# Performance work log

Hardware: AMD Instinct MI355X
Metric: run time of the kernel (lower is better)

## Reference

```python
import jax, jax.numpy as jnp
import numpy as np

B, C, N = 8, 64, 4096
K, M = 20, 8  # neighbors, num_kernel
OUT_C = 64
NEG_SLOPE = 0.2


def setup_inputs() -> dict:
    key = jax.random.key(0)
    k1, k2, k3, k4, k5, k6 = jax.random.split(key, 6)
    x = jax.random.normal(k1, (B, 3, N), dtype=jnp.float32)
    feature = jax.random.normal(k2, (B, C, N), dtype=jnp.float32)
    neigh_indexs = jax.random.randint(k3, (B, N, K), 0, N, dtype=jnp.int64)
    kernels = jax.random.normal(k4, (3, M), dtype=jnp.float32)
    conv_w = jax.random.normal(k5, (OUT_C, C * M), dtype=jnp.float32) * (1.0 / np.sqrt(C * M))
    conv_b = jax.random.normal(k6, (OUT_C,), dtype=jnp.float32) * 0.01
    return {"x": x, "feature": feature, "neigh_indexs": neigh_indexs,
            "kernels": kernels, "conv_w": conv_w, "conv_b": conv_b}


def reference(x, feature, neigh_indexs, kernels, conv_w, conv_b):
    b, c, n = feature.shape
    k = K
    m = kernels.shape[1]
    idx = neigh_indexs[:, :, :k]  # dilation=1 slice, (B,N,K)
    bidx = jnp.arange(b)[:, None, None]

    xt = jnp.transpose(x, (0, 2, 1))            # (B,N,3)
    x_neighs = xt[bidx, idx]                    # (B,N,K,3) irregular gather
    x_rel = x_neighs - x_neighs[:, :, :1, :]    # relative coords to first neighbor

    # kernel projection + one_padding buffer (zeros with [0,0]=1)
    one_pad = jnp.zeros((k, m), dtype=x.dtype).at[0, 0].set(1.0)
    permatrix = jnp.einsum('bnkc,cm->bnkm', x_rel, kernels) + one_pad
    # topkmax: stable softmax over the neighbor axis (soft assignment of
    # neighbors to each of the m kernel slots)
    permatrix = jax.nn.softmax(permatrix, axis=2)  # (B,N,K,M)

    ft = jnp.transpose(feature, (0, 2, 1))      # (B,N,C)
    f_neighs = ft[bidx, idx]                    # (B,N,K,C)
    # feats (B*N,C,K) @ permatrix (B*N,K,M) -> (B*N,C,M); flatten C-major
    agg = jnp.einsum('bnkc,bnkm->bncm', f_neighs, permatrix).reshape(b, n, c * m)

    # BasicConv: 1x1 conv == dense over channel dim, then LeakyReLU(0.2)
    out = agg @ conv_w.T + conv_b               # (B,N,out_c)
    out = jax.nn.leaky_relu(out, NEG_SLOPE)
    out = jnp.transpose(out, (0, 2, 1))         # (B,out_c,N)
    return out + feature                        # residual since in_c == out_c
```

## Files before the change

kernel.cpp:

```cpp
#include <hip/hip_runtime.h>

#define BB 8
#define CC 64
#define NNN 4096
#define KK 20
#define MM 8
#define OC 64
#define CM 512

typedef __attribute__((ext_vector_type(8))) short bf16x8;
typedef __attribute__((ext_vector_type(4))) float f32x4;

__device__ __forceinline__ unsigned short f2bf(float f) {
    union { float f; unsigned int u; } v; v.f = f;
    unsigned int u = v.u;
    return (unsigned short)((u + 0x7FFFu + ((u >> 16) & 1u)) >> 16);
}
__device__ __forceinline__ float bfhi2f(unsigned int u) {
    union { unsigned int u; float f; } v; v.u = u & 0xffff0000u; return v.f;
}
__device__ __forceinline__ float bflo2f(unsigned int u) {
    union { unsigned int u; float f; } v; v.u = u << 16; return v.f;
}

__global__ __launch_bounds__(256) void prep_kernel(const float* __restrict__ feature,
                                                   const float* __restrict__ conv_w,
                                                   unsigned short* __restrict__ ftr,
                                                   unsigned short* __restrict__ Wb) {
    int blk = blockIdx.x;
    int t = threadIdx.x;
    if (blk < 512) {
        __shared__ float tile[64 * 65];
        int b = blk & 7;
        int n0 = (blk >> 3) << 6;
        const float* fb = feature + b * (CC * NNN);
        #pragma unroll
        for (int s = 0; s < 16; ++s) {
            int i = t + s * 256;
            int c = i >> 6, nn = i & 63;
            tile[c * 65 + nn] = fb[c * NNN + n0 + nn];
        }
        __syncthreads();
        unsigned short* fo = ftr + b * (NNN * CC) + n0 * CC;
        #pragma unroll
        for (int s = 0; s < 16; ++s) {
            int i = t + s * 256;
            int n = i >> 6, cc = i & 63;
            fo[n * CC + cc] = f2bf(tile[cc * 65 + n]);
        }
    } else {
        int base = (blk - 512) * 8192;
        #pragma unroll
        for (int s = 0; s < 32; ++s) {
            int i = base + t + s * 256;
            Wb[i] = f2bf(conv_w[i]);
        }
    }
}

__global__ __launch_bounds__(256, 4) void main_kernel(
    const float* __restrict__ x,
    const float* __restrict__ feature,
    const int* __restrict__ nidx,
    const float* __restrict__ kern,
    const float* __restrict__ conv_b,
    const unsigned short* __restrict__ ftr,
    const unsigned short* __restrict__ Wb,
    float* __restrict__ out)
{
    __shared__ __align__(16) union {
        struct {
            int   idx[16 * KK];
            float xn[16 * KK * 3];
            float perm[16 * KK * 10];
        } s;
        unsigned short aggA[16 * 520];
    } u;

    int t = threadIdx.x;
    int blk = blockIdx.x;
    int b = blk & 7;
    int n0 = (blk >> 3) << 4;
    int w = t >> 6, l = t & 63;

    int o = (w << 4) + (l & 15);
    int pq = (l >> 4) << 2;
    float4 fres4 = *(const float4*)(feature + ((size_t)b * CC + o) * NNN + n0 + pq);
    float bias = conv_b[o];
    int m_pre = t & 7;
    float kw0 = kern[m_pre], kw1 = kern[MM + m_pre], kw2 = kern[2 * MM + m_pre];

    const int* nb = nidx + (b * NNN + n0) * KK;
    for (int i = t; i < 16 * KK; i += 256) u.s.idx[i] = nb[i];
    __syncthreads();

    const float* xb = x + b * (3 * NNN);
    float xreg[4];
    int xslot[4];
    #pragma unroll
    for (int s = 0; s < 4; ++s) {
        int i = t + s * 256;
        xslot[s] = i;
        if (i < 960) {
            int p2 = i / 60;
            int rem = i - p2 * 60;
            int k = rem / 3;
            int c = rem - k * 3;
            xreg[s] = xb[c * NNN + u.s.idx[p2 * KK + k]];
        }
    }

    int p = t >> 4;
    int cq = (t & 15) << 2;
    const unsigned short* fb = ftr + (size_t)b * (NNN * CC);
    uint2 fr[KK];
    #pragma unroll
    for (int k = 0; k < KK; ++k)
        fr[k] = *(const uint2*)(fb + (size_t)u.s.idx[p * KK + k] * CC + cq);

    #pragma unroll
    for (int s = 0; s < 4; ++s)
        if (xslot[s] < 960) u.s.xn[xslot[s]] = xreg[s];
    __syncthreads();

    if (t < 128) {
        int pp = t >> 3;
        int m = t & 7;
        const float* xp = &u.s.xn[pp * 60];
        float bx = xp[0], by = xp[1], bz = xp[2];
        float pv[KK];
        #pragma unroll
        for (int k = 0; k < KK; ++k) {
            float dx = xp[k * 3 + 0] - bx;
            float dy = xp[k * 3 + 1] - by;
            float dz = xp[k * 3 + 2] - bz;
            pv[k] = dx * kw0 + dy * kw1 + dz * kw2;
        }
        if (m == 0) pv[0] += 1.0f;
        float mx = pv[0];
        #pragma unroll
        for (int k = 1; k < KK; ++k) mx = fmaxf(mx, pv[k]);
        float sum = 0.f;
        #pragma unroll
        for (int k = 0; k < KK; ++k) { pv[k] = __expf(pv[k] - mx); sum += pv[k]; }
        float inv = 1.0f / sum;
        #pragma unroll
        for (int k = 0; k < KK; ++k) u.s.perm[(pp * KK + k) * 10 + m] = pv[k] * inv;
    }
    __syncthreads();

    float acc[4][MM];
    #pragma unroll
    for (int ci = 0; ci < 4; ++ci)
        #pragma unroll
        for (int m = 0; m < MM; ++m) acc[ci][m] = 0.f;
    #pragma unroll
    for (int k = 0; k < KK; ++k) {
        float fv[4];
        fv[0] = bflo2f(fr[k].x); fv[1] = bfhi2f(fr[k].x);
        fv[2] = bflo2f(fr[k].y); fv[3] = bfhi2f(fr[k].y);
        const float* pr = &u.s.perm[(p * KK + k) * 10];
        float2 q0 = *(const float2*)(pr + 0);
        float2 q1 = *(const float2*)(pr + 2);
        float2 q2 = *(const float2*)(pr + 4);
        float2 q3 = *(const float2*)(pr + 6);
        float pvv[8] = {q0.x, q0.y, q1.x, q1.y, q2.x, q2.y, q3.x, q3.y};
        #pragma unroll
        for (int ci = 0; ci < 4; ++ci)
            #pragma unroll
            for (int m = 0; m < MM; ++m)
                acc[ci][m] += fv[ci] * pvv[m];
    }
    __syncthreads();

    #pragma unroll
    for (int ci = 0; ci < 4; ++ci) {
        union { bf16x8 v; unsigned short s2[8]; } pk;
        #pragma unroll
        for (int m = 0; m < MM; ++m) pk.s2[m] = f2bf(acc[ci][m]);
        *(bf16x8*)&u.aggA[p * 520 + (cq + ci) * MM] = pk.v;
    }
    __syncthreads();

    {
        int row = l & 15;
        int kg = (l >> 4) << 3;
        f32x4 acc2 = {0.f, 0.f, 0.f, 0.f};
        const unsigned short* wrow = Wb + (size_t)o * CM;
        const unsigned short* arow = u.aggA + row * 520;
        #pragma unroll
        for (int s = 0; s < 16; ++s) {
            int k = s * 32 + kg;
            bf16x8 af = *(const bf16x8*)&arow[k];
            bf16x8 bfr = *(const bf16x8*)&wrow[k];
            acc2 = __builtin_amdgcn_mfma_f32_16x16x32_bf16(af, bfr, acc2, 0, 0, 0);
        }
        float4 res;
        #pragma unroll
        for (int r = 0; r < 4; ++r) {
            float v = acc2[r] + bias;
            v = v > 0.f ? v : v * 0.2f;
            ((float*)&res)[r] = v + ((const float*)&fres4)[r];
        }
        *(float4*)(out + ((size_t)b * CC + o) * NNN + n0 + pq) = res;
    }
}

extern "C" void kernel_launch(void* const* d_in, const int* in_sizes, int n_in,
                              void* d_out, int out_size, void* d_ws, size_t ws_size,
                              hipStream_t stream) {
    const float* x        = (const float*)d_in[0];
    const float* feature  = (const float*)d_in[1];
    const int*   nidx     = (const int*)d_in[2];
    const float* kern     = (const float*)d_in[3];
    const float* conv_w   = (const float*)d_in[4];
    const float* conv_b   = (const float*)d_in[5];
    float* out = (float*)d_out;

    unsigned short* ftr = (unsigned short*)d_ws;
    unsigned short* Wb  = (unsigned short*)((char*)d_ws + 4194304);

    prep_kernel<<<516, 256, 0, stream>>>(feature, conv_w, ftr, Wb);
    main_kernel<<<2048, 256, 0, stream>>>(x, feature, nidx, kern, conv_b, ftr, Wb, out);
}
```

Measured before the change: 106.7 us.

## Process 32 points per block, reuse weight fragments across two MFMA tiles

Each block now handles 32 points instead of 16, and the grid is halved. Each thread processes two points, and every conv-weight fragment loaded from global memory feeds two MFMA tiles, which halves weight traffic per point. Neighbor indices are read straight into registers with int4 loads instead of being staged in shared memory, and the second point's feature gather is issued after the softmax stage to overlap latency. The cost is higher register and LDS use, so the occupancy hint drops to 3 blocks, and with 1024 blocks there are fewer waves to hide gather latency.

```diff
diff --git a/kernel.cpp b/kernel.cpp
--- a/kernel.cpp
+++ b/kernel.cpp
@@ -7,6 +7,8 @@
 #define MM 8
 #define OC 64
 #define CM 512
+#define PTS 32
+#define AST 516
 
 typedef __attribute__((ext_vector_type(8))) short bf16x8;
 typedef __attribute__((ext_vector_type(4))) float f32x4;
@@ -58,7 +60,7 @@
     }
 }
 
-__global__ __launch_bounds__(256, 4) void main_kernel(
+__global__ __launch_bounds__(256, 3) void main_kernel(
     const float* __restrict__ x,
     const float* __restrict__ feature,
     const int* __restrict__ nidx,
@@ -70,63 +72,66 @@
 {
     __shared__ __align__(16) union {
         struct {
-            int   idx[16 * KK];
-            float xn[16 * KK * 3];
-            float perm[16 * KK * 10];
+            float xn[PTS * 60];
+            float perm[PTS * KK * 10];
         } s;
-        unsigned short aggA[16 * 520];
+        unsigned short aggA[PTS * AST];
     } u;
 
     int t = threadIdx.x;
     int blk = blockIdx.x;
     int b = blk & 7;
-    int n0 = (blk >> 3) << 4;
+    int n0 = (blk >> 3) << 5;
     int w = t >> 6, l = t & 63;
 
+    const int* nb = nidx + (b * NNN + n0) * KK;
+    const float* xb = x + b * (3 * NNN);
+    const unsigned short* fb = ftr + (size_t)b * (NNN * CC);
+
+    int p0 = t >> 4;
+    int p1 = p0 + 16;
+    int cq = (t & 15) << 2;
     int o = (w << 4) + (l & 15);
-    int pq = (l >> 4) << 2;
-    float4 fres4 = *(const float4*)(feature + ((size_t)b * CC + o) * NNN + n0 + pq);
+    int q = l >> 4;
+
+    float4 fres0 = *(const float4*)(feature + ((size_t)b * CC + o) * NNN + n0 + q * 4);
+    float4 fres1 = *(const float4*)(feature + ((size_t)b * CC + o) * NNN + n0 + 16 + q * 4);
     float bias = conv_b[o];
-    int m_pre = t & 7;
-    float kw0 = kern[m_pre], kw1 = kern[MM + m_pre], kw2 = kern[2 * MM + m_pre];
-
-    const int* nb = nidx + (b * NNN + n0) * KK;
-    for (int i = t; i < 16 * KK; i += 256) u.s.idx[i] = nb[i];
-    __syncthreads();
-
-    const float* xb = x + b * (3 * NNN);
-    float xreg[4];
-    int xslot[4];
-    #pragma unroll
-    for (int s = 0; s < 4; ++s) {
+    int mA = t & 7;
+    float kw0 = kern[mA], kw1 = kern[MM + mA], kw2 = kern[2 * MM + mA];
+
+    int id0[KK];
+    {
+        const int4* nb4 = (const int4*)(nb + p0 * KK);
+        #pragma unroll
+        for (int s = 0; s < 5; ++s) {
+            int4 v = nb4[s];
+            id0[s * 4 + 0] = v.x; id0[s * 4 + 1] = v.y;
+            id0[s * 4 + 2] = v.z; id0[s * 4 + 3] = v.w;
+        }
+    }
+    uint2 fr0[KK];
+    #pragma unroll
+    for (int k = 0; k < KK; ++k)
+        fr0[k] = *(const uint2*)(fb + (size_t)id0[k] * CC + cq);
+
+    #pragma unroll
+    for (int s = 0; s < 8; ++s) {
         int i = t + s * 256;
-        xslot[s] = i;
-        if (i < 960) {
-            int p2 = i / 60;
-            int rem = i - p2 * 60;
+        if (i < PTS * 60) {
+            int p = i / 60;
+            int rem = i - p * 60;
             int k = rem / 3;
             int c = rem - k * 3;
-            xreg[s] = xb[c * NNN + u.s.idx[p2 * KK + k]];
-        }
-    }
-
-    int p = t >> 4;
-    int cq = (t & 15) << 2;
-    const unsigned short* fb = ftr + (size_t)b * (NNN * CC);
-    uint2 fr[KK];
-    #pragma unroll
-    for (int k = 0; k < KK; ++k)
-        fr[k] = *(const uint2*)(fb + (size_t)u.s.idx[p * KK + k] * CC + cq);
-
-    #pragma unroll
-    for (int s = 0; s < 4; ++s)
-        if (xslot[s] < 960) u.s.xn[xslot[s]] = xreg[s];
-    __syncthreads();
-
-    if (t < 128) {
-        int pp = t >> 3;
-        int m = t & 7;
-        const float* xp = &u.s.xn[pp * 60];
+            int idv = nb[p * KK + k];
+            u.s.xn[i] = xb[c * NNN + idv];
+        }
+    }
+    __syncthreads();
+
+    {
+        int pA = t >> 3;
+        const float* xp = &u.s.xn[pA * 60];
         float bx = xp[0], by = xp[1], bz = xp[2];
         float pv[KK];
         #pragma unroll
@@ -136,7 +141,7 @@
             float dz = xp[k * 3 + 2] - bz;
             pv[k] = dx * kw0 + dy * kw1 + dz * kw2;
         }
-        if (m == 0) pv[0] += 1.0f;
+        if (mA == 0) pv[0] += 1.0f;
         float mx = pv[0];
         #pragma unroll
         for (int k = 1; k < KK; ++k) mx = fmaxf(mx, pv[k]);
@@ -145,21 +150,37 @@
         for (int k = 0; k < KK; ++k) { pv[k] = __expf(pv[k] - mx); sum += pv[k]; }
         float inv = 1.0f / sum;
         #pragma unroll
-        for (int k = 0; k < KK; ++k) u.s.perm[(pp * KK + k) * 10 + m] = pv[k] * inv;
-    }
-    __syncthreads();
-
-    float acc[4][MM];
+        for (int k = 0; k < KK; ++k) u.s.perm[(pA * KK + k) * 10 + mA] = pv[k] * inv;
+    }
+    __syncthreads();
+
+    int id1[KK];
+    {
+        const int4* nb4 = (const int4*)(nb + p1 * KK);
+        #pragma unroll
+        for (int s = 0; s < 5; ++s) {
+            int4 v = nb4[s];
+            id1[s * 4 + 0] = v.x; id1[s * 4 + 1] = v.y;
+            id1[s * 4 + 2] = v.z; id1[s * 4 + 3] = v.w;
+        }
+    }
+    uint2 fr1[KK];
+    #pragma unroll
+    for (int k = 0; k < KK; ++k)
+        fr1[k] = *(const uint2*)(fb + (size_t)id1[k] * CC + cq);
+
+    float acc0[4][MM], acc1[4][MM];
     #pragma unroll
     for (int ci = 0; ci < 4; ++ci)
         #pragma unroll
-        for (int m = 0; m < MM; ++m) acc[ci][m] = 0.f;
+        for (int m = 0; m < MM; ++m) { acc0[ci][m] = 0.f; acc1[ci][m] = 0.f; }
+
     #pragma unroll
     for (int k = 0; k < KK; ++k) {
         float fv[4];
-        fv[0] = bflo2f(fr[k].x); fv[1] = bfhi2f(fr[k].x);
-        fv[2] = bflo2f(fr[k].y); fv[3] = bfhi2f(fr[k].y);
-        const float* pr = &u.s.perm[(p * KK + k) * 10];
+        fv[0] = bflo2f(fr0[k].x); fv[1] = bfhi2f(fr0[k].x);
+        fv[2] = bflo2f(fr0[k].y); fv[3] = bfhi2f(fr0[k].y);
+        const float* pr = &u.s.perm[(p0 * KK + k) * 10];
         float2 q0 = *(const float2*)(pr + 0);
         float2 q1 = *(const float2*)(pr + 2);
         float2 q2 = *(const float2*)(pr + 4);
@@ -169,7 +190,24 @@
         for (int ci = 0; ci < 4; ++ci)
             #pragma unroll
             for (int m = 0; m < MM; ++m)
-                acc[ci][m] += fv[ci] * pvv[m];
+                acc0[ci][m] += fv[ci] * pvv[m];
+    }
+    #pragma unroll
+    for (int k = 0; k < KK; ++k) {
+        float fv[4];
+        fv[0] = bflo2f(fr1[k].x); fv[1] = bfhi2f(fr1[k].x);
+        fv[2] = bflo2f(fr1[k].y); fv[3] = bfhi2f(fr1[k].y);
+        const float* pr = &u.s.perm[(p1 * KK + k) * 10];
+        float2 q0 = *(const float2*)(pr + 0);
+        float2 q1 = *(const float2*)(pr + 2);
+        float2 q2 = *(const float2*)(pr + 4);
+        float2 q3 = *(const float2*)(pr + 6);
+        float pvv[8] = {q0.x, q0.y, q1.x, q1.y, q2.x, q2.y, q3.x, q3.y};
+        #pragma unroll
+        for (int ci = 0; ci < 4; ++ci)
+            #pragma unroll
+            for (int m = 0; m < MM; ++m)
+                acc1[ci][m] += fv[ci] * pvv[m];
     }
     __syncthreads();
 
@@ -177,32 +215,44 @@
     for (int ci = 0; ci < 4; ++ci) {
         union { bf16x8 v; unsigned short s2[8]; } pk;
         #pragma unroll
-        for (int m = 0; m < MM; ++m) pk.s2[m] = f2bf(acc[ci][m]);
-        *(bf16x8*)&u.aggA[p * 520 + (cq + ci) * MM] = pk.v;
-    }
-    __syncthreads();
-
-    {
-        int row = l & 15;
-        int kg = (l >> 4) << 3;
-        f32x4 acc2 = {0.f, 0.f, 0.f, 0.f};
+        for (int m = 0; m < MM; ++m) pk.s2[m] = f2bf(acc0[ci][m]);
+        *(bf16x8*)&u.aggA[p0 * AST + (cq + ci) * MM] = pk.v;
+    }
+    #pragma unroll
+    for (int ci = 0; ci < 4; ++ci) {
+        union { bf16x8 v; unsigned short s2[8]; } pk;
+        #pragma unroll
+        for (int m = 0; m < MM; ++m) pk.s2[m] = f2bf(acc1[ci][m]);
+        *(bf16x8*)&u.aggA[p1 * AST + (cq + ci) * MM] = pk.v;
+    }
+    __syncthreads();
+
+    {
+        f32x4 d0 = {0.f, 0.f, 0.f, 0.f};
+        f32x4 d1 = {0.f, 0.f, 0.f, 0.f};
         const unsigned short* wrow = Wb + (size_t)o * CM;
-        const unsigned short* arow = u.aggA + row * 520;
+        const unsigned short* a0 = u.aggA + (l & 15) * AST;
+        const unsigned short* a1 = u.aggA + ((l & 15) + 16) * AST;
         #pragma unroll
         for (int s = 0; s < 16; ++s) {
-            int k = s * 32 + kg;
-            bf16x8 af = *(const bf16x8*)&arow[k];
-            bf16x8 bfr = *(const bf16x8*)&wrow[k];
-            acc2 = __builtin_amdgcn_mfma_f32_16x16x32_bf16(af, bfr, acc2, 0, 0, 0);
-        }
-        float4 res;
+            int koff = s * 32 + q * 8;
+            bf16x8 bB = *(const bf16x8*)&wrow[koff];
+            d0 = __builtin_amdgcn_mfma_f32_16x16x32_bf16(*(const bf16x8*)&a0[koff], bB, d0, 0, 0, 0);
+            d1 = __builtin_amdgcn_mfma_f32_16x16x32_bf16(*(const bf16x8*)&a1[koff], bB, d1, 0, 0, 0);
+        }
+        float* op = out + ((size_t)b * CC + o) * NNN + n0;
+        float4 r0, r1;
         #pragma unroll
         for (int r = 0; r < 4; ++r) {
-            float v = acc2[r] + bias;
-            v = v > 0.f ? v : v * 0.2f;
-            ((float*)&res)[r] = v + ((const float*)&fres4)[r];
-        }
-        *(float4*)(out + ((size_t)b * CC + o) * NNN + n0 + pq) = res;
+            float v0 = d0[r] + bias;
+            v0 = v0 > 0.f ? v0 : v0 * 0.2f;
+            ((float*)&r0)[r] = v0 + ((const float*)&fres0)[r];
+            float v1 = d1[r] + bias;
+            v1 = v1 > 0.f ? v1 : v1 * 0.2f;
+            ((float*)&r1)[r] = v1 + ((const float*)&fres1)[r];
+        }
+        *(float4*)(op + q * 4) = r0;
+        *(float4*)(op + 16 + q * 4) = r1;
     }
 }
 
@@ -221,5 +271,5 @@
     unsigned short* Wb  = (unsigned short*)((char*)d_ws + 4194304);
 
     prep_kernel<<<516, 256, 0, stream>>>(feature, conv_w, ftr, Wb);
-    main_kernel<<<2048, 256, 0, stream>>>(x, feature, nidx, kern, conv_b, ftr, Wb, out);
-}
+    main_kernel<<<1024, 256, 0, stream>>>(x, feature, nidx, kern, conv_b, ftr, Wb, out);
+}
```

Result: slower. 113.1 us (+6.0%).
